# Performance work log

Measured on AMD Instinct MI355X. Metric: run time of the kernel, lower is better.

Reference implementation:

```python
import jax, jax.numpy as jnp
import numpy as np

B, N, NUM = 16384, 512, 3  # batch, num queries, num vanishing points per image


def setup_inputs() -> dict:
    key = jax.random.key(0)
    k1, k2, k3 = jax.random.split(key, 3)
    pred_logits = jax.random.normal(k1, (B, N, 1), jnp.float32)
    pp = jax.random.normal(k2, (B, N, 3), jnp.float32)
    pred_pos = pp / jnp.linalg.norm(pp, axis=-1, keepdims=True)  # unit directions
    vp = jax.random.normal(k3, (B, 3, NUM), jnp.float32)
    vps_unique = vp / jnp.linalg.norm(vp, axis=1, keepdims=True)  # all columns valid (abs-sum > 1e-5)
    return {"pred_logits": pred_logits, "pred_pos": pred_pos, "vps_unique": vps_unique}


def _greedy_select(conf, pos, num):
    # conf: [N,1], pos: [N,3]; greedy angular NMS keeping `num` candidates.
    order = jnp.argsort(-conf[:, 0]).astype(jnp.int32)  # descending confidence
    thresh = jnp.pi / (num + 1)
    ar = jnp.arange(num)
    cand0 = jnp.zeros((num,), jnp.int32).at[0].set(order[0])

    def step(carry, idx):
        cand, count = carry
        sel = pos[cand]                                   # [num,3]
        dots = jnp.minimum(jnp.abs(sel @ pos[idx]), 1.0)  # clip for arccos stability
        ang = jnp.where(ar < count, jnp.arccos(dots), jnp.inf)
        add = (count < num) & (jnp.min(ang) >= thresh)    # torch: skip if dst < pi/(num+1)
        cand = jnp.where(add & (ar == count), idx, cand)
        return (cand, count + add.astype(jnp.int32)), None

    (cand, _), _ = jax.lax.scan(step, (cand0, jnp.int32(1)), order[1:])
    return pos[cand]  # [num,3]


def reference(pred_logits, pred_pos, vps_unique):
    num = vps_unique.shape[2]  # static: all vps columns are valid by construction
    sel = jax.vmap(lambda c, p: _greedy_select(c, p, num))(pred_logits, pred_pos)
    return sel  # [B, num, 3]
```

## Files before the change

### kernel.cpp

```cpp
#include <hip/hip_runtime.h>
#include <math.h>

#define B_TOTAL 16384
#define NQ 512
#define NUM 3

typedef unsigned u32;

__device__ __forceinline__ u32 wave_umax_dpp(u32 v) {
    u32 r = v, t;
    t = (u32)__builtin_amdgcn_update_dpp(0, (int)r, 0x111, 0xF, 0xF, false);
    r = t > r ? t : r;
    t = (u32)__builtin_amdgcn_update_dpp(0, (int)r, 0x112, 0xF, 0xF, false);
    r = t > r ? t : r;
    t = (u32)__builtin_amdgcn_update_dpp(0, (int)r, 0x114, 0xF, 0xF, false);
    r = t > r ? t : r;
    t = (u32)__builtin_amdgcn_update_dpp(0, (int)r, 0x118, 0xF, 0xF, false);
    r = t > r ? t : r;
    t = (u32)__builtin_amdgcn_update_dpp(0, (int)r, 0x142, 0xF, 0xF, false);
    r = t > r ? t : r;
    t = (u32)__builtin_amdgcn_update_dpp(0, (int)r, 0x143, 0xF, 0xF, false);
    r = t > r ? t : r;
    return (u32)__builtin_amdgcn_readlane((int)r, 63);
}

__device__ __forceinline__ u32 wave_umin_dpp(u32 v) {
    u32 r = v, t;
    t = (u32)__builtin_amdgcn_update_dpp(-1, (int)r, 0x111, 0xF, 0xF, false);
    r = t < r ? t : r;
    t = (u32)__builtin_amdgcn_update_dpp(-1, (int)r, 0x112, 0xF, 0xF, false);
    r = t < r ? t : r;
    t = (u32)__builtin_amdgcn_update_dpp(-1, (int)r, 0x114, 0xF, 0xF, false);
    r = t < r ? t : r;
    t = (u32)__builtin_amdgcn_update_dpp(-1, (int)r, 0x118, 0xF, 0xF, false);
    r = t < r ? t : r;
    t = (u32)__builtin_amdgcn_update_dpp(-1, (int)r, 0x142, 0xF, 0xF, false);
    r = t < r ? t : r;
    t = (u32)__builtin_amdgcn_update_dpp(-1, (int)r, 0x143, 0xF, 0xF, false);
    r = t < r ? t : r;
    return (u32)__builtin_amdgcn_readlane((int)r, 63);
}

__global__ __launch_bounds__(256) void greedy_nms_kernel(
    const float* __restrict__ conf,
    const float* __restrict__ pos,
    float* __restrict__ out)
{
    __shared__ float lds[4 * NQ * 3];
    const int lane = threadIdx.x & 63;
    const int wv   = threadIdx.x >> 6;
    const int b    = (blockIdx.x << 2) | wv;

    const float* cb = conf + (size_t)b * NQ;
    const float* pb = pos  + (size_t)b * NQ * 3;
    float* wl = lds + wv * (NQ * 3);

    const float4* pb4 = reinterpret_cast<const float4*>(pb);
    float4 t0 = pb4[0 * 64 + lane];
    float4 t1 = pb4[1 * 64 + lane];
    float4 t2 = pb4[2 * 64 + lane];
    float4 t3 = pb4[3 * 64 + lane];
    float4 t4 = pb4[4 * 64 + lane];
    float4 t5 = pb4[5 * 64 + lane];

    float c[8];
    #pragma unroll
    for (int i = 0; i < 8; ++i) c[i] = cb[i * 64 + lane];

    float4* wl4 = reinterpret_cast<float4*>(wl);
    wl4[0 * 64 + lane] = t0;
    wl4[1 * 64 + lane] = t1;
    wl4[2 * 64 + lane] = t2;
    wl4[3 * 64 + lane] = t3;
    wl4[4 * 64 + lane] = t4;
    wl4[5 * 64 + lane] = t5;

    u32 k[8];
    #pragma unroll
    for (int i = 0; i < 8; ++i) {
        int bi = __float_as_int(c[i]);
        k[i] = (u32)bi ^ ((u32)(bi >> 31) | 0x80000000u);
    }

    __syncthreads();

    auto argmax_dpp = [&](u32& gm_out) -> int {
        u32 m = k[0];
        #pragma unroll
        for (int i = 1; i < 8; ++i) m = k[i] > m ? k[i] : m;
        const u32 gm = wave_umax_dpp(m);
        int im = 8;
        #pragma unroll
        for (int i = 7; i >= 0; --i)
            if (k[i] == gm) im = i;
        const u32 candn = (im < 8) ? (u32)((im << 6) | lane) : 0xFFFFFFFFu;
        const u32 n = wave_umin_dpp(candn);
        gm_out = gm;
        return (int)n;
    };

    auto consume = [&](int n) {
        const int ci = ((n & 63) == lane) ? (n >> 6) : 8;
        #pragma unroll
        for (int i = 0; i < 8; ++i)
            if (ci == i) k[i] = 0u;
    };

    auto get_row = [&](int n, float& x, float& y, float& z) {
        x = wl[3 * n + 0]; y = wl[3 * n + 1]; z = wl[3 * n + 2];
    };

    const float TH  = 0.78539816339744830961f;
    const float CLO = 0.70710478f;
    const float CHI = 0.70710878f;

    auto mask_keys = [&](float px, float py, float pz) {
        #pragma unroll
        for (int i = 0; i < 8; ++i) {
            const int o = 3 * (i * 64 + lane);
            float x = wl[o + 0], y = wl[o + 1], z = wl[o + 2];
            float d = fabsf(x * px + y * py + z * pz);
            bool pass;
            if (d <= CLO)      pass = true;
            else if (d >= CHI) pass = false;
            else               pass = (acosf(fminf(d, 1.f)) >= TH);
            if (!pass) k[i] = 0u;
        }
    };

    u32 gm1;
    const int w1 = argmax_dpp(gm1);
    float p1x, p1y, p1z;
    get_row(w1, p1x, p1y, p1z);
    consume(w1);

    mask_keys(p1x, p1y, p1z);
    u32 gm2;
    const int w2 = argmax_dpp(gm2);

    float o2x, o2y, o2z, o3x, o3y, o3z;
    if (gm2 != 0u) {
        get_row(w2, o2x, o2y, o2z);
        mask_keys(o2x, o2y, o2z);
        u32 gm3;
        const int w3 = argmax_dpp(gm3);
        if (gm3 != 0u) {
            get_row(w3, o3x, o3y, o3z);
        } else {
            get_row(0, o3x, o3y, o3z);
        }
    } else {
        get_row(0, o2x, o2y, o2z);
        o3x = o2x; o3y = o2y; o3z = o2z;
    }

    if (lane == 0) {
        float* ob = out + (size_t)b * 9;
        ob[0] = p1x; ob[1] = p1y; ob[2] = p1z;
        ob[3] = o2x; ob[4] = o2y; ob[5] = o2z;
        ob[6] = o3x; ob[7] = o3y; ob[8] = o3z;
    }
}

extern "C" void kernel_launch(void* const* d_in, const int* in_sizes, int n_in,
                              void* d_out, int out_size, void* d_ws, size_t ws_size,
                              hipStream_t stream) {
    const float* pred_logits = (const float*)d_in[0];
    const float* pred_pos    = (const float*)d_in[1];
    float* out = (float*)d_out;

    const int grid = B_TOTAL / 4;
    greedy_nms_kernel<<<grid, 256, 0, stream>>>(pred_logits, pred_pos, out);
}
```

Measured before the change: 26.37 us.

## Replace full LDS staging of positions with lazy greedy scan fetching candidates on demand

The kernel no longer copies all 512 position vectors per batch into shared memory, and it drops the block barrier. Instead it walks candidates in descending confidence order with wave-wide argmax, fetches only each visited candidate's position from global memory, and stops once two more directions have been accepted. Confidences are now loaded as two float4 per lane, and the key index layout changes to lane*8+slot. This removes most of the position-array traffic, which dominated memory reads. In exchange, each loop step is a serial chain of dependent global loads and wave reductions, whose latency must be hidden by other waves.

```diff
diff --git a/kernel.cpp b/kernel.cpp
--- a/kernel.cpp
+++ b/kernel.cpp
@@ -46,112 +46,94 @@
     const float* __restrict__ pos,
     float* __restrict__ out)
 {
-    __shared__ float lds[4 * NQ * 3];
     const int lane = threadIdx.x & 63;
-    const int wv   = threadIdx.x >> 6;
-    const int b    = (blockIdx.x << 2) | wv;
+    const int b = (blockIdx.x << 2) | (threadIdx.x >> 6);
 
     const float* cb = conf + (size_t)b * NQ;
     const float* pb = pos  + (size_t)b * NQ * 3;
-    float* wl = lds + wv * (NQ * 3);
 
-    const float4* pb4 = reinterpret_cast<const float4*>(pb);
-    float4 t0 = pb4[0 * 64 + lane];
-    float4 t1 = pb4[1 * 64 + lane];
-    float4 t2 = pb4[2 * 64 + lane];
-    float4 t3 = pb4[3 * 64 + lane];
-    float4 t4 = pb4[4 * 64 + lane];
-    float4 t5 = pb4[5 * 64 + lane];
-
-    float c[8];
-    #pragma unroll
-    for (int i = 0; i < 8; ++i) c[i] = cb[i * 64 + lane];
-
-    float4* wl4 = reinterpret_cast<float4*>(wl);
-    wl4[0 * 64 + lane] = t0;
-    wl4[1 * 64 + lane] = t1;
-    wl4[2 * 64 + lane] = t2;
-    wl4[3 * 64 + lane] = t3;
-    wl4[4 * 64 + lane] = t4;
-    wl4[5 * 64 + lane] = t5;
+    const float4* cb4 = reinterpret_cast<const float4*>(cb);
+    const float4 c0 = cb4[lane * 2 + 0];
+    const float4 c1 = cb4[lane * 2 + 1];
+    const float p0x = pb[0], p0y = pb[1], p0z = pb[2];
 
     u32 k[8];
-    #pragma unroll
-    for (int i = 0; i < 8; ++i) {
-        int bi = __float_as_int(c[i]);
-        k[i] = (u32)bi ^ ((u32)(bi >> 31) | 0x80000000u);
+    {
+        float f[8] = {c0.x, c0.y, c0.z, c0.w, c1.x, c1.y, c1.z, c1.w};
+        #pragma unroll
+        for (int s = 0; s < 8; ++s) {
+            int bi = __float_as_int(f[s]);
+            k[s] = (u32)bi ^ ((u32)(bi >> 31) | 0x80000000u);
+        }
     }
-
-    __syncthreads();
 
     auto argmax_dpp = [&](u32& gm_out) -> int {
         u32 m = k[0];
         #pragma unroll
-        for (int i = 1; i < 8; ++i) m = k[i] > m ? k[i] : m;
+        for (int s = 1; s < 8; ++s) m = k[s] > m ? k[s] : m;
         const u32 gm = wave_umax_dpp(m);
         int im = 8;
         #pragma unroll
-        for (int i = 7; i >= 0; --i)
-            if (k[i] == gm) im = i;
-        const u32 candn = (im < 8) ? (u32)((im << 6) | lane) : 0xFFFFFFFFu;
+        for (int s = 7; s >= 0; --s)
+            if (k[s] == gm) im = s;
+        const u32 candn = (im < 8) ? (u32)((lane << 3) | im) : 0xFFFFFFFFu;
         const u32 n = wave_umin_dpp(candn);
         gm_out = gm;
         return (int)n;
     };
 
     auto consume = [&](int n) {
-        const int ci = ((n & 63) == lane) ? (n >> 6) : 8;
+        const int ci = ((n >> 3) == lane) ? (n & 7) : 8;
         #pragma unroll
-        for (int i = 0; i < 8; ++i)
-            if (ci == i) k[i] = 0u;
-    };
-
-    auto get_row = [&](int n, float& x, float& y, float& z) {
-        x = wl[3 * n + 0]; y = wl[3 * n + 1]; z = wl[3 * n + 2];
+        for (int s = 0; s < 8; ++s)
+            if (ci == s) k[s] = 0u;
     };
 
     const float TH  = 0.78539816339744830961f;
     const float CLO = 0.70710478f;
     const float CHI = 0.70710878f;
 
-    auto mask_keys = [&](float px, float py, float pz) {
-        #pragma unroll
-        for (int i = 0; i < 8; ++i) {
-            const int o = 3 * (i * 64 + lane);
-            float x = wl[o + 0], y = wl[o + 1], z = wl[o + 2];
-            float d = fabsf(x * px + y * py + z * pz);
-            bool pass;
-            if (d <= CLO)      pass = true;
-            else if (d >= CHI) pass = false;
-            else               pass = (acosf(fminf(d, 1.f)) >= TH);
-            if (!pass) k[i] = 0u;
-        }
+    auto passv = [&](float ax, float ay, float az,
+                     float px, float py, float pz) -> bool {
+        float d = fabsf(ax * px + ay * py + az * pz);
+        if (d <= CLO) return true;
+        if (d >= CHI) return false;
+        return acosf(fminf(d, 1.f)) >= TH;
     };
 
     u32 gm1;
     const int w1 = argmax_dpp(gm1);
-    float p1x, p1y, p1z;
-    get_row(w1, p1x, p1y, p1z);
     consume(w1);
+    const float p1x = pb[w1 * 3 + 0];
+    const float p1y = pb[w1 * 3 + 1];
+    const float p1z = pb[w1 * 3 + 2];
 
-    mask_keys(p1x, p1y, p1z);
-    u32 gm2;
-    const int w2 = argmax_dpp(gm2);
+    float a1x = 0.f, a1y = 0.f, a1z = 0.f;
+    float o2x = p0x, o2y = p0y, o2z = p0z;
+    float o3x = p0x, o3y = p0y, o3z = p0z;
+    int count = 1;
 
-    float o2x, o2y, o2z, o3x, o3y, o3z;
-    if (gm2 != 0u) {
-        get_row(w2, o2x, o2y, o2z);
-        mask_keys(o2x, o2y, o2z);
-        u32 gm3;
-        const int w3 = argmax_dpp(gm3);
-        if (gm3 != 0u) {
-            get_row(w3, o3x, o3y, o3z);
-        } else {
-            get_row(0, o3x, o3y, o3z);
+    #pragma unroll 1
+    for (int it = 1; it < NQ; ++it) {
+        u32 gm;
+        const int n = argmax_dpp(gm);
+        if (gm == 0u) break;
+        consume(n);
+        const float px = pb[n * 3 + 0];
+        const float py = pb[n * 3 + 1];
+        const float pz = pb[n * 3 + 2];
+        const bool add = passv(p1x, p1y, p1z, px, py, pz) &&
+                         passv(a1x, a1y, a1z, px, py, pz);
+        if (add) {
+            if (count == 1) {
+                o2x = px; o2y = py; o2z = pz;
+                a1x = px; a1y = py; a1z = pz;
+                count = 2;
+            } else {
+                o3x = px; o3y = py; o3z = pz;
+                break;
+            }
         }
-    } else {
-        get_row(0, o2x, o2y, o2z);
-        o3x = o2x; o3y = o2y; o3z = o2z;
     }
 
     if (lane == 0) {
```

After: 26.45 us. No clear change (+0.3%).
